# Optimization experiments

Hardware: AMD Instinct MI355X
Metric: run time of the kernel (lower is better)

Reference implementation:

```python
import jax, jax.numpy as jnp
import numpy as np
from jax import lax

INPUT_DIM = 64
D_MODEL = 128
N_LAYER = 4
LATENT = 128
D_STATE = 16
D_CONV = 4
D_INNER = 2 * D_MODEL          # expand=2 (mamba default)
DT_RANK = (D_MODEL + 15) // 16  # ceil(d_model/16) = 8
B, L = 4, 2048


def setup_inputs() -> dict:
    key = jax.random.key(0)
    ks = jax.random.split(key, 12)
    g = lambda k, s: jax.random.normal(k, s, dtype=jnp.float32) * 0.02
    x = jax.random.normal(ks[0], (B, L, INPUT_DIM), dtype=jnp.float32)
    # S4D-real init for A (standard mamba init)
    A_log = jnp.tile(jnp.log(jnp.arange(1, D_STATE + 1, dtype=jnp.float32)), (N_LAYER, D_INNER, 1))
    return {
        "x": x,
        "W_emb": g(ks[1], (INPUT_DIM, D_MODEL)),
        "b_emb": jnp.zeros((D_MODEL,), jnp.float32),
        "in_proj_w": g(ks[2], (N_LAYER, 2 * D_INNER, D_MODEL)),
        "conv_w": g(ks[3], (N_LAYER, D_INNER, D_CONV)),
        "conv_b": jnp.zeros((N_LAYER, D_INNER), jnp.float32),
        "x_proj_w": g(ks[4], (N_LAYER, DT_RANK + 2 * D_STATE, D_INNER)),
        "dt_proj_w": g(ks[5], (N_LAYER, D_INNER, DT_RANK)),
        "dt_proj_b": jax.random.uniform(ks[6], (N_LAYER, D_INNER), jnp.float32, -4.0, -2.0),
        "A_log": A_log,
        "D_skip": jnp.ones((N_LAYER, D_INNER), jnp.float32),
        "out_proj_w": g(ks[7], (N_LAYER, D_MODEL, D_INNER)),
        "W_lat": g(ks[8], (D_MODEL, LATENT)),
        "b_lat": jnp.zeros((LATENT,), jnp.float32),
    }


def _causal_depthwise_conv(x, w, b):
    # x: [B, L, D_INNER], w: [D_INNER, D_CONV], b: [D_INNER]
    xc = jnp.transpose(x, (0, 2, 1))                       # [B, D, L]
    xc = jnp.pad(xc, ((0, 0), (0, 0), (D_CONV - 1, 0)))    # causal left pad
    out = lax.conv_general_dilated(
        xc, w[:, None, :], window_strides=(1,), padding="VALID",
        dimension_numbers=("NCH", "OIH", "NCH"), feature_group_count=D_INNER)
    return jnp.transpose(out + b[None, :, None], (0, 2, 1))  # [B, L, D]


def _mamba_block(h, in_w, cw, cb, xp_w, dt_w, dt_b, A_log, D_skip, out_w):
    # h: [B, L, D_MODEL]
    xz = jnp.einsum("bld,ed->ble", h, in_w)                 # [B, L, 2*D_INNER]
    u, z = jnp.split(xz, 2, axis=-1)
    u = jax.nn.silu(_causal_depthwise_conv(u, cw, cb))      # [B, L, D_INNER]
    x_dbl = jnp.einsum("bld,ed->ble", u, xp_w)              # [B, L, DT_RANK+2*D_STATE]
    dt, Bm, Cm = jnp.split(x_dbl, [DT_RANK, DT_RANK + D_STATE], axis=-1)
    delta = jax.nn.softplus(jnp.einsum("blr,dr->bld", dt, dt_w) + dt_b)  # [B, L, D_INNER]
    A = -jnp.exp(A_log)                                      # [D_INNER, D_STATE]
    deltaA = jnp.exp(jnp.einsum("bld,dn->bldn", delta, A))   # [B, L, D_INNER, D_STATE]
    deltaBu = jnp.einsum("bld,bln->bldn", delta * u, Bm)

    def step(s, inp):
        dA_t, dBu_t, C_t = inp
        s = dA_t * s + dBu_t                                  # [B, D_INNER, D_STATE]
        y_t = jnp.einsum("bdn,bn->bd", s, C_t)
        return s, y_t

    s0 = jnp.zeros((u.shape[0], D_INNER, D_STATE), u.dtype)
    xs = (jnp.swapaxes(deltaA, 0, 1), jnp.swapaxes(deltaBu, 0, 1), jnp.swapaxes(Cm, 0, 1))
    _, ys = lax.scan(step, s0, xs)                            # [L, B, D_INNER]
    y = jnp.swapaxes(ys, 0, 1) + u * D_skip                   # skip connection D*u
    y = y * jax.nn.silu(z)
    return jnp.einsum("bld,ed->ble", y, out_w)                # [B, L, D_MODEL]


def reference(x, W_emb, b_emb, in_proj_w, conv_w, conv_b, x_proj_w, dt_proj_w,
              dt_proj_b, A_log, D_skip, out_proj_w, W_lat, b_lat):
    h = x @ W_emb + b_emb                                     # [B, L, D_MODEL]
    for i in range(N_LAYER):
        h = _mamba_block(h, in_proj_w[i], conv_w[i], conv_b[i], x_proj_w[i],
                         dt_proj_w[i], dt_proj_b[i], A_log[i], D_skip[i], out_proj_w[i])
    pooled = jnp.mean(h, axis=1)                              # AdaptiveAvgPool1d(1)
    return pooled @ W_lat + b_lat                             # [B, LATENT]
```

## Files before the change

### kernel.cpp

```cpp
#include <hip/hip_runtime.h>
#include <math.h>

#define Bq 4
#define Lq 2048
#define BLq 8192
#define DMq 128
#define DIq 256
#define DSq 16
#define NC2 32
#define TC2 64

__device__ __forceinline__ float siluf(float x){ return x / (1.f + expf(-x)); }
__device__ __forceinline__ float softplusf(float x){
  return (x > 0.f) ? (x + log1pf(expf(-x))) : log1pf(expf(x));
}

__global__ __launch_bounds__(128) void k_embed(const float* __restrict__ x,
    const float* __restrict__ W, const float* __restrict__ bb, float* __restrict__ h){
  int bl = blockIdx.x; int e = threadIdx.x;
  __shared__ float xs[64];
  if (e < 64) xs[e] = x[(size_t)bl*64 + e];
  __syncthreads();
  float acc = bb[e];
  #pragma unroll
  for (int k=0;k<64;k++) acc = fmaf(xs[k], W[k*128 + e], acc);
  h[(size_t)bl*128 + e] = acc;
}

__global__ __launch_bounds__(256) void k_gemm_bt(const float* __restrict__ A,
    const float* __restrict__ W, float* __restrict__ C, int M, int N, int K){
  __shared__ float As[16][68];
  __shared__ float Ws[16][68];
  const int tid = threadIdx.x;
  const int tx = tid & 15, ty = tid >> 4;
  const int lr = tid >> 2, lc = (tid & 3) << 2;
  const int m0 = blockIdx.x << 6, n0 = blockIdx.y << 6;
  float acc[4][4] = {};
  for (int k0 = 0; k0 < K; k0 += 16){
    float4 av = *(const float4*)(A + (size_t)(m0+lr)*K + k0 + lc);
    float4 wv = *(const float4*)(W + (size_t)(n0+lr)*K + k0 + lc);
    As[lc+0][lr]=av.x; As[lc+1][lr]=av.y; As[lc+2][lr]=av.z; As[lc+3][lr]=av.w;
    Ws[lc+0][lr]=wv.x; Ws[lc+1][lr]=wv.y; Ws[lc+2][lr]=wv.z; Ws[lc+3][lr]=wv.w;
    __syncthreads();
    #pragma unroll
    for (int k=0;k<16;k++){
      float4 a = *(const float4*)&As[k][ty<<2];
      float4 w = *(const float4*)&Ws[k][tx<<2];
      acc[0][0]=fmaf(a.x,w.x,acc[0][0]); acc[0][1]=fmaf(a.x,w.y,acc[0][1]);
      acc[0][2]=fmaf(a.x,w.z,acc[0][2]); acc[0][3]=fmaf(a.x,w.w,acc[0][3]);
      acc[1][0]=fmaf(a.y,w.x,acc[1][0]); acc[1][1]=fmaf(a.y,w.y,acc[1][1]);
      acc[1][2]=fmaf(a.y,w.z,acc[1][2]); acc[1][3]=fmaf(a.y,w.w,acc[1][3]);
      acc[2][0]=fmaf(a.z,w.x,acc[2][0]); acc[2][1]=fmaf(a.z,w.y,acc[2][1]);
      acc[2][2]=fmaf(a.z,w.z,acc[2][2]); acc[2][3]=fmaf(a.z,w.w,acc[2][3]);
      acc[3][0]=fmaf(a.w,w.x,acc[3][0]); acc[3][1]=fmaf(a.w,w.y,acc[3][1]);
      acc[3][2]=fmaf(a.w,w.z,acc[3][2]); acc[3][3]=fmaf(a.w,w.w,acc[3][3]);
    }
    __syncthreads();
  }
  #pragma unroll
  for (int i=0;i<4;i++){
    float4 o = make_float4(acc[i][0],acc[i][1],acc[i][2],acc[i][3]);
    *(float4*)(C + (size_t)(m0+(ty<<2)+i)*N + n0 + (tx<<2)) = o;
  }
}

__global__ __launch_bounds__(256) void k_conv(const float* __restrict__ xz,
    const float* __restrict__ cw, const float* __restrict__ cb, float* __restrict__ u){
  int bl = blockIdx.x; int l = bl & 2047; int d = threadIdx.x;
  float4 w = *(const float4*)(cw + d*4);
  float wv[4] = {w.x, w.y, w.z, w.w};
  const float* base = xz + (size_t)bl*512 + d;
  float acc = cb[d];
  #pragma unroll
  for (int j=0;j<4;j++){
    if (l-3+j >= 0) acc = fmaf(base[(j-3)*512], wv[j], acc);
  }
  u[(size_t)bl*256 + d] = siluf(acc);
}

__global__ __launch_bounds__(256) void k_padw(const float* __restrict__ xpw,
    float* __restrict__ xdp){
  int blk = blockIdx.x; int layer = blk >> 6, e = blk & 63;
  int tid = threadIdx.x;
  float v = 0.f;
  if (e < 40) v = xpw[((size_t)layer*40 + e)*256 + tid];
  xdp[((size_t)layer*64 + e)*256 + tid] = v;
}

__global__ __launch_bounds__(256) void k_xg(const float* __restrict__ u,
    const float* __restrict__ xdp, float* __restrict__ xd){
  __shared__ float As[32][34];
  __shared__ float Ws[32][68];
  const int tid = threadIdx.x;
  const int m0 = blockIdx.x << 5;
  const int tm = tid & 15, tn = tid >> 4;
  const int r = tid >> 3, c4 = (tid & 7) << 2;
  float acc[2][4] = {};
  for (int k0=0;k0<256;k0+=32){
    float4 av = *(const float4*)(u + (size_t)(m0+r)*256 + k0 + c4);
    As[c4+0][r]=av.x; As[c4+1][r]=av.y; As[c4+2][r]=av.z; As[c4+3][r]=av.w;
    #pragma unroll
    for (int p=0;p<2;p++){
      int q = tid + p*256;
      int n = q >> 3, wc = (q & 7) << 2;
      float4 wv = *(const float4*)(xdp + (size_t)n*256 + k0 + wc);
      Ws[wc+0][n]=wv.x; Ws[wc+1][n]=wv.y; Ws[wc+2][n]=wv.z; Ws[wc+3][n]=wv.w;
    }
    __syncthreads();
    #pragma unroll
    for (int k=0;k<32;k++){
      float2 a = *(const float2*)&As[k][tm<<1];
      float4 w = *(const float4*)&Ws[k][tn<<2];
      acc[0][0]=fmaf(a.x,w.x,acc[0][0]); acc[0][1]=fmaf(a.x,w.y,acc[0][1]);
      acc[0][2]=fmaf(a.x,w.z,acc[0][2]); acc[0][3]=fmaf(a.x,w.w,acc[0][3]);
      acc[1][0]=fmaf(a.y,w.x,acc[1][0]); acc[1][1]=fmaf(a.y,w.y,acc[1][1]);
      acc[1][2]=fmaf(a.y,w.z,acc[1][2]); acc[1][3]=fmaf(a.y,w.w,acc[1][3]);
    }
    __syncthreads();
  }
  #pragma unroll
  for (int i=0;i<2;i++){
    *(float4*)(xd + (size_t)(m0 + (tm<<1) + i)*64 + (tn<<2)) =
        make_float4(acc[i][0],acc[i][1],acc[i][2],acc[i][3]);
  }
}

__global__ __launch_bounds__(256) void k_delta(const float* __restrict__ xd,
    const float* __restrict__ dtw, const float* __restrict__ dtb,
    float* __restrict__ dlt, float* __restrict__ bc){
  __shared__ float wt[8][256];
  __shared__ float xds[32][8];
  const int tid = threadIdx.x;
  const int row0 = blockIdx.x << 5;
  {
    float4 w0 = *(const float4*)(dtw + tid*8);
    float4 w1 = *(const float4*)(dtw + tid*8 + 4);
    wt[0][tid]=w0.x; wt[1][tid]=w0.y; wt[2][tid]=w0.z; wt[3][tid]=w0.w;
    wt[4][tid]=w1.x; wt[5][tid]=w1.y; wt[6][tid]=w1.z; wt[7][tid]=w1.w;
  }
  if (tid < 64){
    int rr = tid >> 1, cc = (tid & 1) << 2;
    *(float4*)&xds[rr][cc] = *(const float4*)(xd + (size_t)(row0+rr)*64 + cc);
  }
  __syncthreads();
  float bias = dtb[tid];
  for (int rr=0; rr<32; ++rr){
    float acc = bias;
    #pragma unroll
    for (int j=0;j<8;j++) acc = fmaf(xds[rr][j], wt[j][tid], acc);
    dlt[(size_t)(row0+rr)*256 + tid] = softplusf(acc);
  }
  #pragma unroll
  for (int k=0;k<4;k++){
    int idx = k*256 + tid;
    int rr = idx >> 5, cc = idx & 31;
    bc[(size_t)(row0+rr)*32 + cc] = xd[(size_t)(row0+rr)*64 + 8 + cc];
  }
}


__global__ __launch_bounds__(128) void k_scan_a2(const float* __restrict__ dlt,
    const float* __restrict__ u, const float* __restrict__ bc,
    const float* __restrict__ alog, float* __restrict__ sf, float* __restrict__ sd){
  __shared__ float ds_[TC2*32], us_[TC2*32], bs_[TC2*16];
  const int tid = threadIdx.x;
  const int c = blockIdx.x, dg = blockIdx.y, b = blockIdx.z;
  const size_t row0 = (size_t)b*Lq + (size_t)c*TC2;
  {
    const float* dbase = dlt + row0*256 + dg*32;
    const float* ubase = u   + row0*256 + dg*32;
    #pragma unroll
    for (int k=0;k<4;k++){
      int q = tid + k*128;
      int r = q >> 3, c4 = (q & 7) << 2;
      *(float4*)&ds_[r*32 + c4] = *(const float4*)(dbase + (size_t)r*256 + c4);
      *(float4*)&us_[r*32 + c4] = *(const float4*)(ubase + (size_t)r*256 + c4);
    }
    const float* bbase = bc + row0*32;
    #pragma unroll
    for (int k=0;k<2;k++){
      int q = tid + k*128;
      int r = q >> 2, c4 = (q & 3) << 2;
      *(float4*)&bs_[r*16 + c4] = *(const float4*)(bbase + (size_t)r*32 + c4);
    }
  }
  __syncthreads();
  const int lane = tid & 63, w = tid >> 6;
  const int dloc = w*16 + (lane & 15);
  const int nq = (lane >> 4) & 3;
  const int d = dg*32 + dloc;
  float4 al = *(const float4*)(alog + d*16 + nq*4);
  float Av0 = -expf(al.x), Av1 = -expf(al.y), Av2 = -expf(al.z), Av3 = -expf(al.w);
  float s0=0.f,s1=0.f,s2=0.f,s3=0.f, sdl=0.f;
  for (int t=0;t<TC2;t++){
    float de = ds_[t*32 + dloc];
    float uu = us_[t*32 + dloc];
    float du = de*uu;
    float4 Bv = *(const float4*)&bs_[t*16 + (nq<<2)];
    s0 = fmaf(expf(de*Av0), s0, du*Bv.x);
    s1 = fmaf(expf(de*Av1), s1, du*Bv.y);
    s2 = fmaf(expf(de*Av2), s2, du*Bv.z);
    s3 = fmaf(expf(de*Av3), s3, du*Bv.w);
    sdl += de;
  }
  size_t idx = ((size_t)b*NC2 + c)*256 + d;
  *(float4*)(sf + idx*16 + (nq<<2)) = make_float4(s0,s1,s2,s3);
  if (nq==0) sd[idx] = sdl;
}

__global__ __launch_bounds__(256) void k_scan_b2(const float* __restrict__ sf,
    const float* __restrict__ sd, const float* __restrict__ alog, float* __restrict__ si){
  int b = blockIdx.x >> 4, dg = blockIdx.x & 15;
  int tid = threadIdx.x; int n = tid & 15, dl = tid >> 4; int d = dg*16 + dl;
  float Av = -expf(alog[d*16+n]);
  float s = 0.f;
  for (int c=0;c<NC2;c++){
    size_t idx = ((size_t)b*NC2 + c)*256 + d;
    si[idx*16+n] = s;
    s = sf[idx*16+n] + expf(Av * sd[idx]) * s;
  }
}

__global__ __launch_bounds__(128) void k_scan_c2(const float* __restrict__ dlt,
    const float* __restrict__ u, const float* __restrict__ bc,
    const float* __restrict__ xz, const float* __restrict__ si,
    const float* __restrict__ alog, const float* __restrict__ dsk, float* __restrict__ y){
  __shared__ float ds_[TC2*32], us_[TC2*32], bcs_[TC2*32], zs_[TC2*32], ys_[TC2*32];
  const int tid = threadIdx.x;
  const int c = blockIdx.x, dg = blockIdx.y, b = blockIdx.z;
  const size_t row0 = (size_t)b*Lq + (size_t)c*TC2;
  {
    const float* dbase = dlt + row0*256 + dg*32;
    const float* ubase = u   + row0*256 + dg*32;
    const float* zbase = xz  + row0*512 + 256 + dg*32;
    const float* bbase = bc  + row0*32;
    #pragma unroll
    for (int k=0;k<4;k++){
      int q = tid + k*128;
      int r = q >> 3, c4 = (q & 7) << 2;
      *(float4*)&ds_[r*32 + c4]  = *(const float4*)(dbase + (size_t)r*256 + c4);
      *(float4*)&us_[r*32 + c4]  = *(const float4*)(ubase + (size_t)r*256 + c4);
      *(float4*)&zs_[r*32 + c4]  = *(const float4*)(zbase + (size_t)r*512 + c4);
      *(float4*)&bcs_[r*32 + c4] = *(const float4*)(bbase + (size_t)r*32  + c4);
    }
  }
  __syncthreads();
  const int lane = tid & 63, w = tid >> 6;
  const int dloc = w*16 + (lane & 15);
  const int nq = (lane >> 4) & 3;
  const int d = dg*32 + dloc;
  float4 al = *(const float4*)(alog + d*16 + (nq<<2));
  float Av0 = -expf(al.x), Av1 = -expf(al.y), Av2 = -expf(al.z), Av3 = -expf(al.w);
  float Dv = dsk[d];
  size_t idx = ((size_t)b*NC2 + c)*256 + d;
  float4 sv = *(const float4*)(si + idx*16 + (nq<<2));
  float s0 = sv.x, s1 = sv.y, s2 = sv.z, s3 = sv.w;
  for (int t=0;t<TC2;t++){
    float de = ds_[t*32 + dloc];
    float uu = us_[t*32 + dloc];
    float du = de*uu;
    float4 Bv = *(const float4*)&bcs_[t*32 + (nq<<2)];
    float4 Cv = *(const float4*)&bcs_[t*32 + 16 + (nq<<2)];
    s0 = fmaf(expf(de*Av0), s0, du*Bv.x);
    s1 = fmaf(expf(de*Av1), s1, du*Bv.y);
    s2 = fmaf(expf(de*Av2), s2, du*Bv.z);
    s3 = fmaf(expf(de*Av3), s3, du*Bv.w);
    float py = s0*Cv.x + s1*Cv.y + s2*Cv.z + s3*Cv.w;
    py += __shfl_xor(py, 16);
    py += __shfl_xor(py, 32);
    if (nq==0){
      float zz = zs_[t*32 + dloc];
      ys_[t*32 + dloc] = fmaf(uu, Dv, py) * siluf(zz);
    }
  }
  __syncthreads();
  {
    float* ybase = y + row0*256 + dg*32;
    #pragma unroll
    for (int k=0;k<4;k++){
      int q = tid + k*128;
      int r = q >> 3, c4 = (q & 7) << 2;
      *(float4*)(ybase + (size_t)r*256 + c4) = *(const float4*)&ys_[r*32 + c4];
    }
  }
}

__global__ __launch_bounds__(1024) void k_pool(const float* __restrict__ h,
    const float* __restrict__ Wl, const float* __restrict__ bl_, float* __restrict__ out){
  int b = blockIdx.x; int tid = threadIdx.x;
  int e = tid & 127, st = tid >> 7;
  float s = 0.f;
  for (int l = st*256; l < st*256 + 256; ++l) s += h[((size_t)b*2048 + l)*128 + e];
  __shared__ float part[8][128];
  __shared__ float pooled[128];
  part[st][e] = s;
  __syncthreads();
  if (tid < 128){
    float tot = 0.f;
    #pragma unroll
    for (int j=0;j<8;j++) tot += part[j][tid];
    pooled[tid] = tot * (1.f/2048.f);
  }
  __syncthreads();
  if (tid < 128){
    float acc = bl_[tid];
    for (int e2=0;e2<128;e2++) acc = fmaf(pooled[e2], Wl[e2*128 + tid], acc);
    out[b*128 + tid] = acc;
  }
}

extern "C" void kernel_launch(void* const* d_in, const int* in_sizes, int n_in,
                              void* d_out, int out_size, void* d_ws, size_t ws_size,
                              hipStream_t stream){
  const float* x    = (const float*)d_in[0];
  const float* Wem  = (const float*)d_in[1];
  const float* bem  = (const float*)d_in[2];
  const float* inw  = (const float*)d_in[3];
  const float* cw   = (const float*)d_in[4];
  const float* cb   = (const float*)d_in[5];
  const float* xpw  = (const float*)d_in[6];
  const float* dtw  = (const float*)d_in[7];
  const float* dtb  = (const float*)d_in[8];
  const float* alog = (const float*)d_in[9];
  const float* dsk  = (const float*)d_in[10];
  const float* outw = (const float*)d_in[11];
  const float* Wl   = (const float*)d_in[12];
  const float* bl_  = (const float*)d_in[13];
  float* out = (float*)d_out;

  float* p  = (float*)d_ws;
  float* h  = p;  p += (size_t)BLq*128;
  float* xz = p;  p += (size_t)BLq*512;
  float* u  = p;  p += (size_t)BLq*256;
  float* dl = p;  p += (size_t)BLq*256;
  float* bc = p;  p += (size_t)BLq*32;
  float* y  = p;  p += (size_t)BLq*256;
  float* sf = p;  p += (size_t)Bq*NC2*256*16;
  float* sd = p;  p += (size_t)Bq*NC2*256;
  float* si = p;  p += (size_t)Bq*NC2*256*16;
  float* xdp= p;  p += (size_t)4*64*256;
  float* xd = p;  p += (size_t)BLq*64;

  k_padw<<<256, 256, 0, stream>>>(xpw, xdp);
  k_embed<<<BLq, 128, 0, stream>>>(x, Wem, bem, h);
  for (int layer=0; layer<4; ++layer){
    k_gemm_bt<<<dim3(128,8), 256, 0, stream>>>(h, inw + (size_t)layer*512*128, xz, BLq, 512, 128);
    k_conv<<<BLq, 256, 0, stream>>>(xz, cw + (size_t)layer*256*4, cb + (size_t)layer*256, u);
    k_xg<<<256, 256, 0, stream>>>(u, xdp + (size_t)layer*64*256, xd);
    k_delta<<<256, 256, 0, stream>>>(xd, dtw + (size_t)layer*256*8, dtb + (size_t)layer*256,
                                     dl, bc);
    k_scan_a2<<<dim3(NC2,8,Bq), 128, 0, stream>>>(dl, u, bc, alog + (size_t)layer*4096, sf, sd);
    k_scan_b2<<<64, 256, 0, stream>>>(sf, sd, alog + (size_t)layer*4096, si);
    k_scan_c2<<<dim3(NC2,8,Bq), 128, 0, stream>>>(dl, u, bc, xz, si, alog + (size_t)layer*4096,
                                                  dsk + (size_t)layer*256, y);
    k_gemm_bt<<<dim3(128,2), 256, 0, stream>>>(y, outw + (size_t)layer*128*256, h, BLq, 128, 256);
  }
  k_pool<<<Bq, 1024, 0, stream>>>(h, Wl, bl_, out);
}
```

Baseline: 617.4 us.

## Use split-bf16 MFMA GEMMs for in/out projections with bf16 hi/lo operand storage

```diff
diff --git a/kernel.cpp b/kernel.cpp
--- a/kernel.cpp
+++ b/kernel.cpp
@@ -10,13 +10,35 @@
 #define NC2 32
 #define TC2 64
 
+typedef short short8 __attribute__((ext_vector_type(8)));
+typedef float f32x4 __attribute__((ext_vector_type(4)));
+
 __device__ __forceinline__ float siluf(float x){ return x / (1.f + expf(-x)); }
 __device__ __forceinline__ float softplusf(float x){
   return (x > 0.f) ? (x + log1pf(expf(-x))) : log1pf(expf(x));
 }
+__device__ __forceinline__ unsigned short f2bf(float v){
+  unsigned int u = __float_as_uint(v);
+  return (unsigned short)((u + 0x7FFFu + ((u >> 16) & 1u)) >> 16);
+}
+__device__ __forceinline__ float bf2f(unsigned short h){
+  return __uint_as_float(((unsigned int)h) << 16);
+}
+
+__global__ __launch_bounds__(256) void k_split(const float* __restrict__ in,
+    unsigned short* __restrict__ hi, unsigned short* __restrict__ lo, int n){
+  int i = blockIdx.x*256 + threadIdx.x;
+  if (i < n){
+    float v = in[i];
+    unsigned short h = f2bf(v);
+    hi[i] = h;
+    lo[i] = f2bf(v - bf2f(h));
+  }
+}
 
 __global__ __launch_bounds__(128) void k_embed(const float* __restrict__ x,
-    const float* __restrict__ W, const float* __restrict__ bb, float* __restrict__ h){
+    const float* __restrict__ W, const float* __restrict__ bb, float* __restrict__ h,
+    unsigned short* __restrict__ hhi, unsigned short* __restrict__ hlo){
   int bl = blockIdx.x; int e = threadIdx.x;
   __shared__ float xs[64];
   if (e < 64) xs[e] = x[(size_t)bl*64 + e];
@@ -24,43 +46,71 @@
   float acc = bb[e];
   #pragma unroll
   for (int k=0;k<64;k++) acc = fmaf(xs[k], W[k*128 + e], acc);
-  h[(size_t)bl*128 + e] = acc;
-}
-
-__global__ __launch_bounds__(256) void k_gemm_bt(const float* __restrict__ A,
-    const float* __restrict__ W, float* __restrict__ C, int M, int N, int K){
-  __shared__ float As[16][68];
-  __shared__ float Ws[16][68];
+  size_t idx = (size_t)bl*128 + e;
+  h[idx] = acc;
+  unsigned short hb = f2bf(acc);
+  hhi[idx] = hb;
+  hlo[idx] = f2bf(acc - bf2f(hb));
+}
+
+__global__ __launch_bounds__(256) void k_mfma_bt(
+    const unsigned short* __restrict__ Ahi, const unsigned short* __restrict__ Alo,
+    const unsigned short* __restrict__ Whi, const unsigned short* __restrict__ Wlo,
+    float* __restrict__ C, unsigned short* __restrict__ Chi, unsigned short* __restrict__ Clo,
+    int M, int N, int K){
   const int tid = threadIdx.x;
-  const int tx = tid & 15, ty = tid >> 4;
-  const int lr = tid >> 2, lc = (tid & 3) << 2;
-  const int m0 = blockIdx.x << 6, n0 = blockIdx.y << 6;
-  float acc[4][4] = {};
-  for (int k0 = 0; k0 < K; k0 += 16){
-    float4 av = *(const float4*)(A + (size_t)(m0+lr)*K + k0 + lc);
-    float4 wv = *(const float4*)(W + (size_t)(n0+lr)*K + k0 + lc);
-    As[lc+0][lr]=av.x; As[lc+1][lr]=av.y; As[lc+2][lr]=av.z; As[lc+3][lr]=av.w;
-    Ws[lc+0][lr]=wv.x; Ws[lc+1][lr]=wv.y; Ws[lc+2][lr]=wv.z; Ws[lc+3][lr]=wv.w;
-    __syncthreads();
-    #pragma unroll
-    for (int k=0;k<16;k++){
-      float4 a = *(const float4*)&As[k][ty<<2];
-      float4 w = *(const float4*)&Ws[k][tx<<2];
-      acc[0][0]=fmaf(a.x,w.x,acc[0][0]); acc[0][1]=fmaf(a.x,w.y,acc[0][1]);
-      acc[0][2]=fmaf(a.x,w.z,acc[0][2]); acc[0][3]=fmaf(a.x,w.w,acc[0][3]);
-      acc[1][0]=fmaf(a.y,w.x,acc[1][0]); acc[1][1]=fmaf(a.y,w.y,acc[1][1]);
-      acc[1][2]=fmaf(a.y,w.z,acc[1][2]); acc[1][3]=fmaf(a.y,w.w,acc[1][3]);
-      acc[2][0]=fmaf(a.z,w.x,acc[2][0]); acc[2][1]=fmaf(a.z,w.y,acc[2][1]);
-      acc[2][2]=fmaf(a.z,w.z,acc[2][2]); acc[2][3]=fmaf(a.z,w.w,acc[2][3]);
-      acc[3][0]=fmaf(a.w,w.x,acc[3][0]); acc[3][1]=fmaf(a.w,w.y,acc[3][1]);
-      acc[3][2]=fmaf(a.w,w.z,acc[3][2]); acc[3][3]=fmaf(a.w,w.w,acc[3][3]);
-    }
-    __syncthreads();
-  }
+  const int l = tid & 63, w = tid >> 6;
+  const int wr = w >> 1, wc = w & 1;
+  const int l15 = l & 15;
+  const int ko = (l >> 4) << 3;
+  const int m0 = blockIdx.x << 7;
+  const int n0 = blockIdx.y << 6;
+  const int arow = m0 + wr*64 + l15;
+  const int wrow = n0 + wc*32 + l15;
+  f32x4 acc[4][2] = {};
+  for (int kk = 0; kk < K; kk += 32){
+    short8 ah[4], al[4], wh[2], wl[2];
+    #pragma unroll
+    for (int t=0;t<4;t++){
+      size_t off = (size_t)(arow + t*16)*K + kk + ko;
+      ah[t] = *(const short8*)(Ahi + off);
+      al[t] = *(const short8*)(Alo + off);
+    }
+    #pragma unroll
+    for (int s=0;s<2;s++){
+      size_t off = (size_t)(wrow + s*16)*K + kk + ko;
+      wh[s] = *(const short8*)(Whi + off);
+      wl[s] = *(const short8*)(Wlo + off);
+    }
+    #pragma unroll
+    for (int t=0;t<4;t++){
+      #pragma unroll
+      for (int s=0;s<2;s++){
+        acc[t][s] = __builtin_amdgcn_mfma_f32_16x16x32_bf16(ah[t], wh[s], acc[t][s], 0,0,0);
+        acc[t][s] = __builtin_amdgcn_mfma_f32_16x16x32_bf16(ah[t], wl[s], acc[t][s], 0,0,0);
+        acc[t][s] = __builtin_amdgcn_mfma_f32_16x16x32_bf16(al[t], wh[s], acc[t][s], 0,0,0);
+      }
+    }
+  }
+  const int r0 = (l >> 4) << 2;
   #pragma unroll
-  for (int i=0;i<4;i++){
-    float4 o = make_float4(acc[i][0],acc[i][1],acc[i][2],acc[i][3]);
-    *(float4*)(C + (size_t)(m0+(ty<<2)+i)*N + n0 + (tx<<2)) = o;
+  for (int t=0;t<4;t++){
+    #pragma unroll
+    for (int s=0;s<2;s++){
+      #pragma unroll
+      for (int r=0;r<4;r++){
+        int row = m0 + wr*64 + t*16 + r0 + r;
+        int col = n0 + wc*32 + s*16 + l15;
+        size_t idx = (size_t)row*N + col;
+        float v = acc[t][s][r];
+        C[idx] = v;
+        if (Chi){
+          unsigned short hb = f2bf(v);
+          Chi[idx] = hb;
+          Clo[idx] = f2bf(v - bf2f(hb));
+        }
+      }
+    }
   }
 }
 
@@ -157,7 +207,6 @@
     bc[(size_t)(row0+rr)*32 + cc] = xd[(size_t)(row0+rr)*64 + 8 + cc];
   }
 }
-
 
 __global__ __launch_bounds__(128) void k_scan_a2(const float* __restrict__ dlt,
     const float* __restrict__ u, const float* __restrict__ bc,
@@ -224,7 +273,8 @@
 __global__ __launch_bounds__(128) void k_scan_c2(const float* __restrict__ dlt,
     const float* __restrict__ u, const float* __restrict__ bc,
     const float* __restrict__ xz, const float* __restrict__ si,
-    const float* __restrict__ alog, const float* __restrict__ dsk, float* __restrict__ y){
+    const float* __restrict__ alog, const float* __restrict__ dsk,
+    unsigned short* __restrict__ yhi, unsigned short* __restrict__ ylo){
   __shared__ float ds_[TC2*32], us_[TC2*32], bcs_[TC2*32], zs_[TC2*32], ys_[TC2*32];
   const int tid = threadIdx.x;
   const int c = blockIdx.x, dg = blockIdx.y, b = blockIdx.z;
@@ -275,12 +325,20 @@
   }
   __syncthreads();
   {
-    float* ybase = y + row0*256 + dg*32;
+    unsigned short* yh = yhi + row0*256 + dg*32;
+    unsigned short* yl = ylo + row0*256 + dg*32;
     #pragma unroll
     for (int k=0;k<4;k++){
       int q = tid + k*128;
       int r = q >> 3, c4 = (q & 7) << 2;
-      *(float4*)(ybase + (size_t)r*256 + c4) = *(const float4*)&ys_[r*32 + c4];
+      float4 v = *(const float4*)&ys_[r*32 + c4];
+      ushort4 h4, l4;
+      h4.x = f2bf(v.x); l4.x = f2bf(v.x - bf2f(h4.x));
+      h4.y = f2bf(v.y); l4.y = f2bf(v.y - bf2f(h4.y));
+      h4.z = f2bf(v.z); l4.z = f2bf(v.z - bf2f(h4.z));
+      h4.w = f2bf(v.w); l4.w = f2bf(v.w - bf2f(h4.w));
+      *(ushort4*)(yh + (size_t)r*256 + c4) = h4;
+      *(ushort4*)(yl + (size_t)r*256 + c4) = l4;
     }
   }
 }
@@ -334,17 +392,29 @@
   float* u  = p;  p += (size_t)BLq*256;
   float* dl = p;  p += (size_t)BLq*256;
   float* bc = p;  p += (size_t)BLq*32;
-  float* y  = p;  p += (size_t)BLq*256;
   float* sf = p;  p += (size_t)Bq*NC2*256*16;
   float* sd = p;  p += (size_t)Bq*NC2*256;
   float* si = p;  p += (size_t)Bq*NC2*256*16;
   float* xdp= p;  p += (size_t)4*64*256;
   float* xd = p;  p += (size_t)BLq*64;
-
+  unsigned short* q = (unsigned short*)p;
+  unsigned short* wihi = q; q += (size_t)4*512*128;
+  unsigned short* wilo = q; q += (size_t)4*512*128;
+  unsigned short* wohi = q; q += (size_t)4*128*256;
+  unsigned short* wolo = q; q += (size_t)4*128*256;
+  unsigned short* hhi  = q; q += (size_t)BLq*128;
+  unsigned short* hlo  = q; q += (size_t)BLq*128;
+  unsigned short* yhi  = q; q += (size_t)BLq*256;
+  unsigned short* ylo  = q; q += (size_t)BLq*256;
+
+  k_split<<<1024, 256, 0, stream>>>(inw, wihi, wilo, 4*512*128);
+  k_split<<<512, 256, 0, stream>>>(outw, wohi, wolo, 4*128*256);
   k_padw<<<256, 256, 0, stream>>>(xpw, xdp);
-  k_embed<<<BLq, 128, 0, stream>>>(x, Wem, bem, h);
+  k_embed<<<BLq, 128, 0, stream>>>(x, Wem, bem, h, hhi, hlo);
   for (int layer=0; layer<4; ++layer){
-    k_gemm_bt<<<dim3(128,8), 256, 0, stream>>>(h, inw + (size_t)layer*512*128, xz, BLq, 512, 128);
+    k_mfma_bt<<<dim3(64,8), 256, 0, stream>>>(hhi, hlo,
+        wihi + (size_t)layer*512*128, wilo + (size_t)layer*512*128,
+        xz, nullptr, nullptr, BLq, 512, 128);
     k_conv<<<BLq, 256, 0, stream>>>(xz, cw + (size_t)layer*256*4, cb + (size_t)layer*256, u);
     k_xg<<<256, 256, 0, stream>>>(u, xdp + (size_t)layer*64*256, xd);
     k_delta<<<256, 256, 0, stream>>>(xd, dtw + (size_t)layer*256*8, dtb + (size_t)layer*256,
@@ -352,8 +422,10 @@
     k_scan_a2<<<dim3(NC2,8,Bq), 128, 0, stream>>>(dl, u, bc, alog + (size_t)layer*4096, sf, sd);
     k_scan_b2<<<64, 256, 0, stream>>>(sf, sd, alog + (size_t)layer*4096, si);
     k_scan_c2<<<dim3(NC2,8,Bq), 128, 0, stream>>>(dl, u, bc, xz, si, alog + (size_t)layer*4096,
-                                                  dsk + (size_t)layer*256, y);
-    k_gemm_bt<<<dim3(128,2), 256, 0, stream>>>(y, outw + (size_t)layer*128*256, h, BLq, 128, 256);
+                                                  dsk + (size_t)layer*256, yhi, ylo);
+    k_mfma_bt<<<dim3(64,2), 256, 0, stream>>>(yhi, ylo,
+        wohi + (size_t)layer*128*256, wolo + (size_t)layer*128*256,
+        h, hhi, hlo, BLq, 128, 256);
   }
   k_pool<<<Bq, 1024, 0, stream>>>(h, Wl, bl_, out);
 }
```

After: 626.2 us. Within noise of the previous version (+1.4%).
